# Optimization experiments

Measured on AMD Instinct MI355X. Metric: run time of the kernel, lower is better.

Reference implementation:

```python
import jax, jax.numpy as jnp
import numpy as np
import math

BN_EPS = 1e-5
LOG20 = math.log(20.0)

def conv1x1(w, x):
    # w: [O, C], x: [B, C, N] -> [B, O, N]
    return jnp.einsum('oc,bcn->bon', w, x)

def bn_silu(x, g, b, m, v):
    # inference-mode BatchNorm1d over channel dim, then SiLU
    y = (x - m[None, :, None]) * (g / jnp.sqrt(v + BN_EPS))[None, :, None] + b[None, :, None]
    return y * jax.nn.sigmoid(y)

def setup_inputs() -> dict:
    key = jax.random.key(0)
    ks = jax.random.split(key, 16)
    B, N, M = 8, 4096, 4096
    f32 = jnp.float32
    d = {
        'pcd_f': jax.random.normal(ks[0], (B, 1152, N), f32),
        'img_f': jax.random.normal(ks[1], (B, 1024, M), f32),
        'q_w': jax.random.normal(ks[2], (1024, 1152), f32) * 0.02,
        'k_w': jax.random.normal(ks[3], (1024, 1024), f32) * 0.02,
        'v_w': jax.random.normal(ks[4], (1024, 1024), f32) * 0.02,
        'skip_w': jax.random.normal(ks[5], (1024, 1152), f32) * 0.02,
        'c1_w': jax.random.normal(ks[6], (256, 1024), f32) * 0.03,
        'bn1_g': jnp.ones((256,), f32),
        'bn1_b': jnp.zeros((256,), f32),
        'bn1_m': jax.random.normal(ks[7], (256,), f32) * 0.1,
        'bn1_v': jnp.ones((256,), f32) + 0.1 * jax.random.uniform(ks[8], (256,)),
        'c2_w': jax.random.normal(ks[9], (64, 256), f32) * 0.06,
        'bn2_g': jnp.ones((64,), f32),
        'bn2_b': jnp.zeros((64,), f32),
        'bn2_m': jax.random.normal(ks[10], (64,), f32) * 0.1,
        'bn2_v': jnp.ones((64,), f32) + 0.1 * jax.random.uniform(ks[11], (64,)),
        'c3_w': jax.random.normal(ks[12], (1, 64), f32) * 0.1,
        'c3_b': jnp.zeros((1,), f32),
    }
    return d

def reference(pcd_f, img_f, q_w, k_w, v_w, skip_w, c1_w, bn1_g, bn1_b, bn1_m, bn1_v,
              c2_w, bn2_g, bn2_b, bn2_m, bn2_v, c3_w, c3_b):
    q = conv1x1(q_w, pcd_f)                       # [B, 1024, N]
    k = conv1x1(k_w, img_f)                       # [B, 1024, M]
    v = conv1x1(v_w, img_f)                       # [B, 1024, M]
    scale = math.sqrt(q.shape[1])                 # sqrt(C) = 32
    energy = jnp.einsum('bcn,bcm->bnm', q, k) / scale
    attn = jax.nn.softmax(energy, axis=-1)        # [B, N, M]
    x = jnp.einsum('bnm,bcm->bcn', attn, v)       # [B, 1024, N]
    x = conv1x1(skip_w, pcd_f) + x
    x = bn_silu(conv1x1(c1_w, x), bn1_g, bn1_b, bn1_m, bn1_v)   # [B, 256, N]
    x = bn_silu(conv1x1(c2_w, x), bn2_g, bn2_b, bn2_m, bn2_v)   # [B, 64, N]
    x = conv1x1(c3_w, x) + c3_b[None, :, None]    # [B, 1, N]
    x = x[:, 0, :]                                # squeeze channel -> [B, N]
    return jax.nn.sigmoid(x * LOG20)              # 1/(1+20^-x)
```

## Files before the change

### kernel.cpp

```cpp
#include <hip/hip_runtime.h>

#define LOG20F 2.9957322735539909f
#define AS1 __attribute__((address_space(1)))
#define AS3 __attribute__((address_space(3)))

typedef __attribute__((ext_vector_type(4))) short short4v;
typedef __attribute__((ext_vector_type(8))) short short8;
typedef __attribute__((ext_vector_type(8))) __bf16 bf16x8;
typedef __attribute__((ext_vector_type(4))) float f32x4;

__device__ __forceinline__ short f2bf(float f) {
  unsigned u = __float_as_uint(f);
  u = u + 0x7fffu + ((u >> 16) & 1u);
  return (short)(u >> 16);
}
__device__ __forceinline__ float bf2f(short s) {
  return __uint_as_float(((unsigned)(unsigned short)s) << 16);
}

__device__ __forceinline__ void xcd_map(int& bx, int& by, int& bz) {
  int gx = gridDim.x, gy = gridDim.y;
  int nwg = gx * gy * (int)gridDim.z;
  int lin = bx + gx * (by + gy * bz);
  int q = nwg >> 3, r = nwg & 7;
  int xcd = lin & 7, idx = lin >> 3;
  int wg = (xcd < r ? xcd * (q + 1) : r * (q + 1) + (xcd - r) * q) + idx;
  int per_z = gx * gy;
  bz = wg / per_z;
  int rz = wg - bz * per_z;
  if ((gx & 3) == 0 && (gy & 3) == 0) {
    int nstx = gx >> 2;
    int st = rz >> 4, w = rz & 15;
    bx = ((st % nstx) << 2) + (w & 3);
    by = ((st / nstx) << 2) + (w >> 2);
  } else {
    bx = rz % gx;
    by = rz / gx;
  }
}

template <int EPI>
__global__ __launch_bounds__(512, 2) void gemm8(
    const short* __restrict__ A, const short* __restrict__ B,
    short* __restrict__ C, const short* __restrict__ addp,
    int K, int lda, int ldb, int ldc, int ldadd,
    long abatch, long bbatch, long cbatch, long addbatch, float scale)
{
  __shared__ __align__(16) short lA[2][256 * 64];
  __shared__ __align__(16) short lB[2][256 * 64];

  int bx = blockIdx.x, by = blockIdx.y, bz = blockIdx.z;
  xcd_map(bx, by, bz);

  const int tid = threadIdx.x;
  const int lane = tid & 63, wid = tid >> 6;
  const int wr = wid >> 2, wc = wid & 3;

  const long bm = (long)bx * 256, bn = (long)by * 256;
  const short* Ab = A + (long)bz * abatch + bm * lda;
  const short* Bb = B + (long)bz * bbatch + bn * ldb;

  f32x4 acc[8][4] = {};

  const int NKT = K >> 6;

  auto stageA = [&](int buf, int kt) {
    int k0 = kt << 6;
#pragma unroll
    for (int i = 0; i < 4; ++i) {
      int idx = i * 512 + tid;
      int row = idx >> 3, ch = idx & 7;
      int chs = ch ^ (row & 7);
      __builtin_amdgcn_global_load_lds(
          (const AS1 void*)(Ab + (long)row * lda + k0 + chs * 8),
          (AS3 void*)(&lA[buf][row * 64 + ch * 8]), 16, 0, 0);
    }
  };
  auto stageB = [&](int buf, int kt) {
    int k0 = kt << 6;
#pragma unroll
    for (int i = 0; i < 4; ++i) {
      int idx = i * 512 + tid;
      int row = idx >> 3, ch = idx & 7;
      int chs = ch ^ (row & 7);
      __builtin_amdgcn_global_load_lds(
          (const AS1 void*)(Bb + (long)row * ldb + k0 + chs * 8),
          (AS3 void*)(&lB[buf][row * 64 + ch * 8]), 16, 0, 0);
    }
  };

  const int rr = lane & 15, cl = lane >> 4;
  bf16x8 bfr[4][2], af[4][2];

  auto loadA2 = [&](int buf, int h) {
#pragma unroll
    for (int f = 0; f < 4; ++f) {
      int row = wr * 128 + h * 64 + f * 16 + rr;
#pragma unroll
      for (int kk = 0; kk < 2; ++kk) {
        int pch = (kk * 4 + cl) ^ (row & 7);
        af[f][kk] = *(const bf16x8*)&lA[buf][row * 64 + pch * 8];
      }
    }
  };
  auto loadB2 = [&](int buf) {
#pragma unroll
    for (int ni = 0; ni < 4; ++ni) {
      int row = wc * 64 + ni * 16 + rr;
#pragma unroll
      for (int kk = 0; kk < 2; ++kk) {
        int pch = (kk * 4 + cl) ^ (row & 7);
        bfr[ni][kk] = *(const bf16x8*)&lB[buf][row * 64 + pch * 8];
      }
    }
  };

#define BAR() __builtin_amdgcn_s_barrier()
#define LGKM0() asm volatile("s_waitcnt lgkmcnt(0)" ::: "memory")
#define MFMA_H(h)                                                        \
  do {                                                                   \
    __builtin_amdgcn_s_setprio(1);                                       \
    _Pragma("unroll")                                                    \
    for (int f = 0; f < 4; ++f)                                          \
      _Pragma("unroll")                                                  \
      for (int ni = 0; ni < 4; ++ni)                                     \
        _Pragma("unroll")                                                \
        for (int kk = 0; kk < 2; ++kk)                                   \
          acc[(h) * 4 + f][ni] = __builtin_amdgcn_mfma_f32_16x16x32_bf16(\
              af[f][kk], bfr[ni][kk], acc[(h) * 4 + f][ni], 0, 0, 0);    \
    __builtin_amdgcn_s_setprio(0);                                       \
  } while (0)

  stageB(0, 0); stageA(0, 0); stageB(1, 1);
  asm volatile("s_waitcnt vmcnt(4)" ::: "memory");
  BAR();

  for (int t2 = 0; t2 < NKT; t2 += 2) {
    const bool more = (t2 + 2 < NKT);
    stageA(1, t2 + 1);
    loadB2(0); loadA2(0, 0);
    BAR(); LGKM0(); MFMA_H(0); BAR();
    if (more) stageB(0, t2 + 2);
    loadA2(0, 1);
    if (more) { asm volatile("s_waitcnt vmcnt(4)" ::: "memory"); }
    else      { asm volatile("s_waitcnt vmcnt(0)" ::: "memory"); }
    BAR(); LGKM0(); MFMA_H(1); BAR();
    if (more) stageA(0, t2 + 2);
    loadB2(1); loadA2(1, 0);
    BAR(); LGKM0(); MFMA_H(0); BAR();
    if (more) stageB(1, t2 + 3);
    loadA2(1, 1);
    if (more) { asm volatile("s_waitcnt vmcnt(4)" ::: "memory"); }
    else      { asm volatile("s_waitcnt vmcnt(0)" ::: "memory"); }
    BAR(); LGKM0(); MFMA_H(1); BAR();
  }
#undef BAR
#undef LGKM0
#undef MFMA_H

#pragma unroll
  for (int mi = 0; mi < 8; ++mi) {
    long row0 = bm + wr * 128 + (mi >> 2) * 64 + (mi & 3) * 16 + (cl << 2);
#pragma unroll
    for (int ni = 0; ni < 4; ++ni) {
      long col = bn + wc * 64 + ni * 16 + rr;
#pragma unroll
      for (int r = 0; r < 4; ++r) {
        long off = (long)bz * cbatch + (row0 + r) * ldc + col;
        float v = acc[mi][ni][r] * scale;
        if constexpr (EPI == 1)
          v += bf2f(addp[(long)bz * addbatch + (row0 + r) * ldadd + col]);
        C[off] = f2bf(v);
      }
    }
  }
}

__device__ __forceinline__ int swz32(int row, int ch) {
  return row * 32 + ((ch ^ ((row >> 1) & 3)) << 3);
}

template <int BM, int BN, int WR, int WC, int EPI>
__global__ __launch_bounds__(WR * WC * 64, 4) void gemm_bt(
    const short* __restrict__ A, const short* __restrict__ B,
    short* __restrict__ C, const short* __restrict__ addp,
    const float* __restrict__ sc, const float* __restrict__ sh,
    int K, int lda, int ldb, int ldc,
    long abatch, long bbatch, long cbatch, float scale)
{
  constexpr int NTH = WR * WC * 64;
  constexpr int WM = BM / WR, WN = BN / WC;
  constexpr int MR = WM / 16, NR = WN / 16;
  constexpr int CA = (BM * 4) / NTH, CB = (BN * 4) / NTH;

  __shared__ __align__(16) short lA[2][BM * 32];
  __shared__ __align__(16) short lB[2][BN * 32];

  int bx = blockIdx.x, by = blockIdx.y, bz = blockIdx.z;
  xcd_map(bx, by, bz);

  const int tid = threadIdx.x;
  const int lane = tid & 63, wid = tid >> 6;
  const int wr = wid / WC, wc = wid % WC;

  const long bm = (long)bx * BM, bn = (long)by * BN;
  const short* Ab = A + (long)bz * abatch + bm * lda;
  const short* Bb = B + (long)bz * bbatch + bn * ldb;

  f32x4 acc[MR][NR] = {};

  auto stage = [&](int buf, int k0) {
#pragma unroll
    for (int i = 0; i < CA; ++i) {
      int idx = i * NTH + tid, row = idx >> 2, ch = idx & 3;
      int chs = ch ^ ((row >> 1) & 3);
      __builtin_amdgcn_global_load_lds(
          (const AS1 void*)(Ab + (long)row * lda + k0 + chs * 8),
          (AS3 void*)(&lA[buf][idx * 8]), 16, 0, 0);
    }
#pragma unroll
    for (int i = 0; i < CB; ++i) {
      int idx = i * NTH + tid, row = idx >> 2, ch = idx & 3;
      int chs = ch ^ ((row >> 1) & 3);
      __builtin_amdgcn_global_load_lds(
          (const AS1 void*)(Bb + (long)row * ldb + k0 + chs * 8),
          (AS3 void*)(&lB[buf][idx * 8]), 16, 0, 0);
    }
  };

  const int NT = K >> 5;
  stage(0, 0);
  __syncthreads();
  int cur = 0;
  for (int t = 0; t < NT; ++t) {
    if (t + 1 < NT) stage(cur ^ 1, (t + 1) << 5);
    const int ch = lane >> 4, rrow = lane & 15;
    bf16x8 af[MR], bfr[NR];
#pragma unroll
    for (int mi = 0; mi < MR; ++mi) {
      int row = wr * WM + mi * 16 + rrow;
      af[mi] = *(const bf16x8*)&lA[cur][swz32(row, ch)];
    }
#pragma unroll
    for (int ni = 0; ni < NR; ++ni) {
      int row = wc * WN + ni * 16 + rrow;
      bfr[ni] = *(const bf16x8*)&lB[cur][swz32(row, ch)];
    }
    __builtin_amdgcn_s_setprio(1);
#pragma unroll
    for (int mi = 0; mi < MR; ++mi)
#pragma unroll
      for (int ni = 0; ni < NR; ++ni)
        acc[mi][ni] = __builtin_amdgcn_mfma_f32_16x16x32_bf16(
            af[mi], bfr[ni], acc[mi][ni], 0, 0, 0);
    __builtin_amdgcn_s_setprio(0);
    __syncthreads();
    cur ^= 1;
  }

#pragma unroll
  for (int mi = 0; mi < MR; ++mi) {
    long row0 = bm + wr * WM + mi * 16 + ((lane >> 4) << 2);
#pragma unroll
    for (int ni = 0; ni < NR; ++ni) {
      long col = bn + wc * WN + ni * 16 + (lane & 15);
#pragma unroll
      for (int r = 0; r < 4; ++r) {
        long off = (long)bz * cbatch + (row0 + r) * ldc + col;
        float v = acc[mi][ni][r] * scale;
        if constexpr (EPI == 1) v += bf2f(addp[off]);
        if constexpr (EPI == 2) {
          float y = v * sc[col] + sh[col];
          v = y / (1.f + __expf(-y));
        }
        C[off] = f2bf(v);
      }
    }
  }
}

__global__ __launch_bounds__(256) void transpose_cvt(
    const float* __restrict__ in, short* __restrict__ out, int C, int N)
{
  __shared__ float tile[32][33];
  int n0 = blockIdx.x * 32, c0 = blockIdx.y * 32;
  long z = (long)blockIdx.z * C * N;
  int tx = threadIdx.x & 31, ty = threadIdx.x >> 5;
#pragma unroll
  for (int r = 0; r < 4; ++r) {
    int cc = ty + r * 8;
    tile[cc][tx] = in[z + (long)(c0 + cc) * N + n0 + tx];
  }
  __syncthreads();
#pragma unroll
  for (int r = 0; r < 4; ++r) {
    int nn = ty + r * 8;
    out[z + (long)(n0 + nn) * C + c0 + tx] = f2bf(tile[tx][nn]);
  }
}

__global__ __launch_bounds__(256) void cvt_bf16(
    const float* __restrict__ in, short* __restrict__ out, long n)
{
  long i = ((long)blockIdx.x * 256 + threadIdx.x) * 4;
  if (i >= n) return;
  const float* p = in + i;
  short4v s;
  s[0] = f2bf(p[0]); s[1] = f2bf(p[1]); s[2] = f2bf(p[2]); s[3] = f2bf(p[3]);
  *(short4v*)(out + i) = s;
}

__global__ void bn_prep(const float* g1, const float* b1, const float* m1, const float* v1,
                        const float* g2, const float* b2, const float* m2, const float* v2,
                        float* s1, float* t1, float* s2, float* t2)
{
  int i = threadIdx.x;
  if (i < 256) { float s = g1[i] * rsqrtf(v1[i] + 1e-5f); s1[i] = s; t1[i] = b1[i] - m1[i] * s; }
  if (i < 64)  { float s = g2[i] * rsqrtf(v2[i] + 1e-5f); s2[i] = s; t2[i] = b2[i] - m2[i] * s; }
}

__global__ __launch_bounds__(256) void softmax_row(short* __restrict__ a)
{
  __shared__ float rm[4], rs[4];
  long row = blockIdx.x;
  short* p = a + row * 4096;
  int tid = threadIdx.x;
  short8 v0 = *(short8*)(p + tid * 16);
  short8 v1 = *(short8*)(p + tid * 16 + 8);
  float f[16];
#pragma unroll
  for (int j = 0; j < 8; ++j) { f[j] = bf2f(v0[j]); f[8 + j] = bf2f(v1[j]); }
  float m = f[0];
#pragma unroll
  for (int j = 1; j < 16; ++j) m = fmaxf(m, f[j]);
  for (int o = 32; o > 0; o >>= 1) m = fmaxf(m, __shfl_xor(m, o));
  if ((tid & 63) == 0) rm[tid >> 6] = m;
  __syncthreads();
  m = fmaxf(fmaxf(rm[0], rm[1]), fmaxf(rm[2], rm[3]));
  float s = 0.f;
#pragma unroll
  for (int j = 0; j < 16; ++j) { f[j] = __expf(f[j] - m); s += f[j]; }
  for (int o = 32; o > 0; o >>= 1) s += __shfl_xor(s, o);
  if ((tid & 63) == 0) rs[tid >> 6] = s;
  __syncthreads();
  s = rs[0] + rs[1] + rs[2] + rs[3];
  float inv = 1.f / s;
#pragma unroll
  for (int j = 0; j < 8; ++j) { v0[j] = f2bf(f[j] * inv); v1[j] = f2bf(f[8 + j] * inv); }
  *(short8*)(p + tid * 16) = v0;
  *(short8*)(p + tid * 16 + 8) = v1;
}

__global__ __launch_bounds__(256) void c3_out(
    const short* __restrict__ y2, const float* __restrict__ w,
    const float* __restrict__ bias, float* __restrict__ o, int total)
{
  int i = blockIdx.x * 256 + threadIdx.x;
  if (i >= total) return;
  const short8* r = (const short8*)(y2 + (long)i * 64);
  float acc = 0.f;
#pragma unroll
  for (int j0 = 0; j0 < 8; ++j0) {
    short8 v = r[j0];
#pragma unroll
    for (int j = 0; j < 8; ++j) acc += bf2f(v[j]) * w[j0 * 8 + j];
  }
  acc += bias[0];
  float x = acc * LOG20F;
  o[i] = 1.f / (1.f + __expf(-x));
}

extern "C" void kernel_launch(void* const* d_in, const int* in_sizes, int n_in,
                              void* d_out, int out_size, void* d_ws, size_t ws_size,
                              hipStream_t stream) {
  const float* pcd  = (const float*)d_in[0];
  const float* img  = (const float*)d_in[1];
  const float* qw   = (const float*)d_in[2];
  const float* kw   = (const float*)d_in[3];
  const float* vw   = (const float*)d_in[4];
  const float* skw  = (const float*)d_in[5];
  const float* c1w  = (const float*)d_in[6];
  const float* bn1g = (const float*)d_in[7];
  const float* bn1b = (const float*)d_in[8];
  const float* bn1m = (const float*)d_in[9];
  const float* bn1v = (const float*)d_in[10];
  const float* c2w  = (const float*)d_in[11];
  const float* bn2g = (const float*)d_in[12];
  const float* bn2b = (const float*)d_in[13];
  const float* bn2m = (const float*)d_in[14];
  const float* bn2v = (const float*)d_in[15];
  const float* c3w  = (const float*)d_in[16];
  const float* c3b  = (const float*)d_in[17];
  float* out = (float*)d_out;

  char* ws = (char*)d_ws;
  const long QS  = 4096L * 1024;
  const long QS2 = 4096L * 2048;
  const long ES  = 4096L * 4096;
  const size_t ALGN = 256;
  auto align_up = [&](size_t x) { return (x + ALGN - 1) & ~(ALGN - 1); };

  size_t oPcd  = 0;
  size_t oImg  = align_up(oPcd + 8L * 4096 * 1152 * 2);
  size_t oQsk  = align_up(oImg + 8L * 4096 * 1024 * 2);
  size_t oKt   = align_up(oQsk + 8L * QS2 * 2);
  size_t oV    = align_up(oKt  + 8L * QS * 2);
  size_t oWqs  = align_up(oV   + 8L * QS * 2);
  size_t oWk   = align_up(oWqs + 2048L * 1152 * 2);
  size_t oWv   = align_up(oWk + 1024L * 1024 * 2);
  size_t oC1   = align_up(oWv + 1024L * 1024 * 2);
  size_t oC2   = align_up(oC1 + 256L * 1024 * 2);
  size_t oS1   = align_up(oC2 + 64L * 256 * 2);
  size_t oT1   = align_up(oS1 + 256 * 4);
  size_t oS2   = align_up(oT1 + 256 * 4);
  size_t oT2   = align_up(oS2 + 64 * 4);
  size_t oEnd  = align_up(oT2 + 64 * 4);

  short* pcdT  = (short*)(ws + oPcd);
  short* imgT  = (short*)(ws + oImg);
  short* qsk   = (short*)(ws + oQsk);
  short* kt    = (short*)(ws + oKt);
  short* vbuf  = (short*)(ws + oV);
  short* wqsk  = (short*)(ws + oWqs);
  short* wkb   = (short*)(ws + oWk);
  short* wvb   = (short*)(ws + oWv);
  short* c1b   = (short*)(ws + oC1);
  short* c2b   = (short*)(ws + oC2);
  float* s1 = (float*)(ws + oS1); float* t1 = (float*)(ws + oT1);
  float* s2 = (float*)(ws + oS2); float* t2 = (float*)(ws + oT2);

  int NB; short *attn, *xt;
  if (ws_size >= oEnd + (size_t)(8L * ES * 2) + (size_t)(8L * QS * 2)) {
    NB = 8; attn = (short*)(ws + oEnd); xt = (short*)(ws + align_up(oEnd + 8L * ES * 2));
  } else if (ws_size >= oEnd + (size_t)(8L * QS * 2)) {
    NB = 4; attn = (short*)(ws + 0); xt = (short*)(ws + oEnd);
  } else {
    NB = 2; attn = imgT; xt = pcdT;
  }
  short* y1t = qsk;
  short* y2t = kt;

  cvt_bf16<<<dim3(1152), 256, 0, stream>>>(qw,  wqsk,                 1024L * 1152);
  cvt_bf16<<<dim3(1152), 256, 0, stream>>>(skw, wqsk + 1024L * 1152,  1024L * 1152);
  cvt_bf16<<<dim3(1024), 256, 0, stream>>>(kw,  wkb,  1024L * 1024);
  cvt_bf16<<<dim3(1024), 256, 0, stream>>>(vw,  wvb,  1024L * 1024);
  cvt_bf16<<<dim3(256),  256, 0, stream>>>(c1w, c1b,  256L * 1024);
  cvt_bf16<<<dim3(16),   256, 0, stream>>>(c2w, c2b,  64L * 256);
  bn_prep<<<1, 256, 0, stream>>>(bn1g, bn1b, bn1m, bn1v, bn2g, bn2b, bn2m, bn2v,
                                 s1, t1, s2, t2);
  transpose_cvt<<<dim3(128, 36, 8), 256, 0, stream>>>(pcd, pcdT, 1152, 4096);
  transpose_cvt<<<dim3(128, 32, 8), 256, 0, stream>>>(img, imgT, 1024, 4096);

  gemm8<0><<<dim3(16, 8, 8), 512, 0, stream>>>(
      pcdT, wqsk, qsk, nullptr,
      1152, 1152, 1152, 2048, 0, 4096L * 1152, 0, QS2, 0, 1.f);
  gemm8<0><<<dim3(16, 4, 8), 512, 0, stream>>>(
      imgT, wkb, kt, nullptr,
      1024, 1024, 1024, 1024, 0, QS, 0, QS, 0, 1.f);
  gemm8<0><<<dim3(4, 16, 8), 512, 0, stream>>>(
      wvb, imgT, vbuf, nullptr,
      1024, 1024, 1024, 4096, 0, 0, QS, QS, 0, 1.f);

  for (int b0 = 0; b0 < 8; b0 += NB) {
    gemm8<0><<<dim3(16, 16, NB), 512, 0, stream>>>(
        qsk + (long)b0 * QS2, kt + (long)b0 * QS, attn, nullptr,
        1024, 2048, 1024, 4096, 0, QS2, QS, ES, 0, 0.03125f);
    softmax_row<<<dim3(4096 * NB), 256, 0, stream>>>(attn);
    gemm8<1><<<dim3(16, 4, NB), 512, 0, stream>>>(
        attn, vbuf + (long)b0 * QS, xt + (long)b0 * QS,
        qsk + (long)b0 * QS2 + 1024,
        4096, 4096, 4096, 1024, 2048, ES, QS, QS, QS2, 1.f);
  }

  gemm_bt<128, 128, 2, 2, 2><<<dim3(32, 2, 8), 256, 0, stream>>>(
      xt, c1b, y1t, nullptr, s1, t1,
      1024, 1024, 1024, 256, QS, 0, 4096L * 256, 1.f);
  gemm_bt<128, 64, 4, 1, 2><<<dim3(32, 1, 8), 256, 0, stream>>>(
      y1t, c2b, y2t, nullptr, s2, t2,
      256, 256, 256, 64, 4096L * 256, 0, 4096L * 64, 1.f);
  c3_out<<<dim3(128), 256, 0, stream>>>(y2t, c3w, c3b, out, 32768);

  (void)in_sizes; (void)n_in; (void)out_size; (void)ws_size;
}
```

Measured before the change: 1.111 ms.

## Fuse softmax into QK and PV GEMM epilogues and pad leading dimensions

Drops the separate softmax kernel. The QK^T GEMM epilogue now writes exp(scaled energy) and adds row sums into a global buffer through shared and global atomics, and the PV GEMM divides by the row sum in its epilogue. This saves a full read and write pass over the attention matrix. The max subtraction is skipped, which relies on the logits staying small enough not to overflow. Leading dimensions are also padded (e.g. 4128, 1056, 2080) to avoid LDS and channel conflicts, and the NB=8 path is removed so batches are always processed in chunks.

```diff
diff --git a/kernel.cpp b/kernel.cpp
--- a/kernel.cpp
+++ b/kernel.cpp
@@ -43,11 +43,13 @@
 __global__ __launch_bounds__(512, 2) void gemm8(
     const short* __restrict__ A, const short* __restrict__ B,
     short* __restrict__ C, const short* __restrict__ addp,
+    float* __restrict__ rs,
     int K, int lda, int ldb, int ldc, int ldadd,
     long abatch, long bbatch, long cbatch, long addbatch, float scale)
 {
   __shared__ __align__(16) short lA[2][256 * 64];
   __shared__ __align__(16) short lB[2][256 * 64];
+  __shared__ float rsum_l[256];
 
   int bx = blockIdx.x, by = blockIdx.y, bz = blockIdx.z;
   xcd_map(bx, by, bz);
@@ -158,19 +160,49 @@
 #undef LGKM0
 #undef MFMA_H
 
-#pragma unroll
-  for (int mi = 0; mi < 8; ++mi) {
-    long row0 = bm + wr * 128 + (mi >> 2) * 64 + (mi & 3) * 16 + (cl << 2);
-#pragma unroll
-    for (int ni = 0; ni < 4; ++ni) {
-      long col = bn + wc * 64 + ni * 16 + rr;
+  if constexpr (EPI == 2) {
+    if (tid < 256) rsum_l[tid] = 0.f;
+    __syncthreads();
+#pragma unroll
+    for (int mi = 0; mi < 8; ++mi) {
+      int lrow0 = wr * 128 + (mi >> 2) * 64 + (mi & 3) * 16 + (cl << 2);
 #pragma unroll
       for (int r = 0; r < 4; ++r) {
-        long off = (long)bz * cbatch + (row0 + r) * ldc + col;
-        float v = acc[mi][ni][r] * scale;
-        if constexpr (EPI == 1)
-          v += bf2f(addp[(long)bz * addbatch + (row0 + r) * ldadd + col]);
-        C[off] = f2bf(v);
+        float part = 0.f;
+#pragma unroll
+        for (int ni = 0; ni < 4; ++ni) {
+          long col = bn + wc * 64 + ni * 16 + rr;
+          float e = __expf(acc[mi][ni][r] * scale);
+          C[(long)bz * cbatch + (bm + lrow0 + r) * ldc + col] = f2bf(e);
+          part += e;
+        }
+        atomicAdd(&rsum_l[lrow0 + r], part);
+      }
+    }
+    __syncthreads();
+    if (tid < 256) atomicAdd(&rs[(long)bz * 4096 + bm + tid], rsum_l[tid]);
+  } else {
+#pragma unroll
+    for (int mi = 0; mi < 8; ++mi) {
+      long row0 = bm + wr * 128 + (mi >> 2) * 64 + (mi & 3) * 16 + (cl << 2);
+      float inv[4];
+      if constexpr (EPI == 1) {
+#pragma unroll
+        for (int r = 0; r < 4; ++r)
+          inv[r] = 1.f / rs[(long)bz * 4096 + row0 + r];
+      }
+#pragma unroll
+      for (int ni = 0; ni < 4; ++ni) {
+        long col = bn + wc * 64 + ni * 16 + rr;
+#pragma unroll
+        for (int r = 0; r < 4; ++r) {
+          long off = (long)bz * cbatch + (row0 + r) * ldc + col;
+          float v = acc[mi][ni][r] * scale;
+          if constexpr (EPI == 1)
+            v = v * inv[r] +
+                bf2f(addp[(long)bz * addbatch + (row0 + r) * ldadd + col]);
+          C[off] = f2bf(v);
+        }
       }
     }
   }
@@ -280,22 +312,23 @@
 }
 
 __global__ __launch_bounds__(256) void transpose_cvt(
-    const float* __restrict__ in, short* __restrict__ out, int C, int N)
+    const float* __restrict__ in, short* __restrict__ out, int C, int N, int ldo)
 {
   __shared__ float tile[32][33];
   int n0 = blockIdx.x * 32, c0 = blockIdx.y * 32;
-  long z = (long)blockIdx.z * C * N;
+  long zi = (long)blockIdx.z * C * N;
+  long zo = (long)blockIdx.z * (long)N * ldo;
   int tx = threadIdx.x & 31, ty = threadIdx.x >> 5;
 #pragma unroll
   for (int r = 0; r < 4; ++r) {
     int cc = ty + r * 8;
-    tile[cc][tx] = in[z + (long)(c0 + cc) * N + n0 + tx];
+    tile[cc][tx] = in[zi + (long)(c0 + cc) * N + n0 + tx];
   }
   __syncthreads();
 #pragma unroll
   for (int r = 0; r < 4; ++r) {
     int nn = ty + r * 8;
-    out[z + (long)(n0 + nn) * C + c0 + tx] = f2bf(tile[tx][nn]);
+    out[zo + (long)(n0 + nn) * ldo + c0 + tx] = f2bf(tile[tx][nn]);
   }
 }
 
@@ -319,36 +352,10 @@
   if (i < 64)  { float s = g2[i] * rsqrtf(v2[i] + 1e-5f); s2[i] = s; t2[i] = b2[i] - m2[i] * s; }
 }
 
-__global__ __launch_bounds__(256) void softmax_row(short* __restrict__ a)
-{
-  __shared__ float rm[4], rs[4];
-  long row = blockIdx.x;
-  short* p = a + row * 4096;
-  int tid = threadIdx.x;
-  short8 v0 = *(short8*)(p + tid * 16);
-  short8 v1 = *(short8*)(p + tid * 16 + 8);
-  float f[16];
-#pragma unroll
-  for (int j = 0; j < 8; ++j) { f[j] = bf2f(v0[j]); f[8 + j] = bf2f(v1[j]); }
-  float m = f[0];
-#pragma unroll
-  for (int j = 1; j < 16; ++j) m = fmaxf(m, f[j]);
-  for (int o = 32; o > 0; o >>= 1) m = fmaxf(m, __shfl_xor(m, o));
-  if ((tid & 63) == 0) rm[tid >> 6] = m;
-  __syncthreads();
-  m = fmaxf(fmaxf(rm[0], rm[1]), fmaxf(rm[2], rm[3]));
-  float s = 0.f;
-#pragma unroll
-  for (int j = 0; j < 16; ++j) { f[j] = __expf(f[j] - m); s += f[j]; }
-  for (int o = 32; o > 0; o >>= 1) s += __shfl_xor(s, o);
-  if ((tid & 63) == 0) rs[tid >> 6] = s;
-  __syncthreads();
-  s = rs[0] + rs[1] + rs[2] + rs[3];
-  float inv = 1.f / s;
-#pragma unroll
-  for (int j = 0; j < 8; ++j) { v0[j] = f2bf(f[j] * inv); v1[j] = f2bf(f[8 + j] * inv); }
-  *(short8*)(p + tid * 16) = v0;
-  *(short8*)(p + tid * 16 + 8) = v1;
+__global__ __launch_bounds__(256) void zerof(float* __restrict__ p, int n)
+{
+  int i = blockIdx.x * 256 + threadIdx.x;
+  if (i < n) p[i] = 0.f;
 }
 
 __global__ __launch_bounds__(256) void c3_out(
@@ -393,19 +400,22 @@
   const float* c3b  = (const float*)d_in[17];
   float* out = (float*)d_out;
 
+  const int QLD = 2080, KLD = 1056, ALD = 4128, VLD = 4128, Y1LD = 288;
+  const long QS2 = 4096L * QLD;
+  const long QS  = 4096L * KLD;
+  const long VBS = 1024L * VLD;
+  const long ES  = 4096L * ALD;
+
   char* ws = (char*)d_ws;
-  const long QS  = 4096L * 1024;
-  const long QS2 = 4096L * 2048;
-  const long ES  = 4096L * 4096;
   const size_t ALGN = 256;
   auto align_up = [&](size_t x) { return (x + ALGN - 1) & ~(ALGN - 1); };
 
   size_t oPcd  = 0;
   size_t oImg  = align_up(oPcd + 8L * 4096 * 1152 * 2);
-  size_t oQsk  = align_up(oImg + 8L * 4096 * 1024 * 2);
+  size_t oQsk  = align_up(oImg + 8L * 4096 * KLD * 2);
   size_t oKt   = align_up(oQsk + 8L * QS2 * 2);
   size_t oV    = align_up(oKt  + 8L * QS * 2);
-  size_t oWqs  = align_up(oV   + 8L * QS * 2);
+  size_t oWqs  = align_up(oV   + 8L * VBS * 2);
   size_t oWk   = align_up(oWqs + 2048L * 1152 * 2);
   size_t oWv   = align_up(oWk + 1024L * 1024 * 2);
   size_t oC1   = align_up(oWv + 1024L * 1024 * 2);
@@ -414,7 +424,8 @@
   size_t oT1   = align_up(oS1 + 256 * 4);
   size_t oS2   = align_up(oT1 + 256 * 4);
   size_t oT2   = align_up(oS2 + 64 * 4);
-  size_t oEnd  = align_up(oT2 + 64 * 4);
+  size_t oRs   = align_up(oT2 + 64 * 4);
+  size_t oEnd  = align_up(oRs + 8L * 4096 * 4);
 
   short* pcdT  = (short*)(ws + oPcd);
   short* imgT  = (short*)(ws + oImg);
@@ -428,56 +439,57 @@
   short* c2b   = (short*)(ws + oC2);
   float* s1 = (float*)(ws + oS1); float* t1 = (float*)(ws + oT1);
   float* s2 = (float*)(ws + oS2); float* t2 = (float*)(ws + oT2);
+  float* rsum = (float*)(ws + oRs);
 
   int NB; short *attn, *xt;
-  if (ws_size >= oEnd + (size_t)(8L * ES * 2) + (size_t)(8L * QS * 2)) {
-    NB = 8; attn = (short*)(ws + oEnd); xt = (short*)(ws + align_up(oEnd + 8L * ES * 2));
-  } else if (ws_size >= oEnd + (size_t)(8L * QS * 2)) {
+  if (ws_size >= oEnd + (size_t)(8L * QS * 2)) {
     NB = 4; attn = (short*)(ws + 0); xt = (short*)(ws + oEnd);
   } else {
-    NB = 2; attn = imgT; xt = pcdT;
+    NB = 2; attn = (short*)(ws + 0);
+    xt = (short*)(ws + align_up((size_t)(2L * ES * 2)));
   }
   short* y1t = qsk;
   short* y2t = kt;
 
-  cvt_bf16<<<dim3(1152), 256, 0, stream>>>(qw,  wqsk,                 1024L * 1152);
-  cvt_bf16<<<dim3(1152), 256, 0, stream>>>(skw, wqsk + 1024L * 1152,  1024L * 1152);
+  cvt_bf16<<<dim3(1152), 256, 0, stream>>>(qw,  wqsk,                1024L * 1152);
+  cvt_bf16<<<dim3(1152), 256, 0, stream>>>(skw, wqsk + 1024L * 1152, 1024L * 1152);
   cvt_bf16<<<dim3(1024), 256, 0, stream>>>(kw,  wkb,  1024L * 1024);
   cvt_bf16<<<dim3(1024), 256, 0, stream>>>(vw,  wvb,  1024L * 1024);
   cvt_bf16<<<dim3(256),  256, 0, stream>>>(c1w, c1b,  256L * 1024);
   cvt_bf16<<<dim3(16),   256, 0, stream>>>(c2w, c2b,  64L * 256);
   bn_prep<<<1, 256, 0, stream>>>(bn1g, bn1b, bn1m, bn1v, bn2g, bn2b, bn2m, bn2v,
                                  s1, t1, s2, t2);
-  transpose_cvt<<<dim3(128, 36, 8), 256, 0, stream>>>(pcd, pcdT, 1152, 4096);
-  transpose_cvt<<<dim3(128, 32, 8), 256, 0, stream>>>(img, imgT, 1024, 4096);
+  zerof<<<dim3(128), 256, 0, stream>>>(rsum, 8 * 4096);
+  transpose_cvt<<<dim3(128, 36, 8), 256, 0, stream>>>(pcd, pcdT, 1152, 4096, 1152);
+  transpose_cvt<<<dim3(128, 32, 8), 256, 0, stream>>>(img, imgT, 1024, 4096, KLD);
 
   gemm8<0><<<dim3(16, 8, 8), 512, 0, stream>>>(
-      pcdT, wqsk, qsk, nullptr,
-      1152, 1152, 1152, 2048, 0, 4096L * 1152, 0, QS2, 0, 1.f);
+      pcdT, wqsk, qsk, nullptr, nullptr,
+      1152, 1152, 1152, QLD, 0, 4096L * 1152, 0, QS2, 0, 1.f);
   gemm8<0><<<dim3(16, 4, 8), 512, 0, stream>>>(
-      imgT, wkb, kt, nullptr,
-      1024, 1024, 1024, 1024, 0, QS, 0, QS, 0, 1.f);
+      imgT, wkb, kt, nullptr, nullptr,
+      1024, KLD, 1024, KLD, 0, QS, 0, QS, 0, 1.f);
   gemm8<0><<<dim3(4, 16, 8), 512, 0, stream>>>(
-      wvb, imgT, vbuf, nullptr,
-      1024, 1024, 1024, 4096, 0, 0, QS, QS, 0, 1.f);
+      wvb, imgT, vbuf, nullptr, nullptr,
+      1024, 1024, KLD, VLD, 0, 0, QS, VBS, 0, 1.f);
 
   for (int b0 = 0; b0 < 8; b0 += NB) {
-    gemm8<0><<<dim3(16, 16, NB), 512, 0, stream>>>(
+    gemm8<2><<<dim3(16, 16, NB), 512, 0, stream>>>(
         qsk + (long)b0 * QS2, kt + (long)b0 * QS, attn, nullptr,
-        1024, 2048, 1024, 4096, 0, QS2, QS, ES, 0, 0.03125f);
-    softmax_row<<<dim3(4096 * NB), 256, 0, stream>>>(attn);
+        rsum + (long)b0 * 4096,
+        1024, QLD, KLD, ALD, 0, QS2, QS, ES, 0, 0.03125f);
     gemm8<1><<<dim3(16, 4, NB), 512, 0, stream>>>(
-        attn, vbuf + (long)b0 * QS, xt + (long)b0 * QS,
-        qsk + (long)b0 * QS2 + 1024,
-        4096, 4096, 4096, 1024, 2048, ES, QS, QS, QS2, 1.f);
+        attn, vbuf + (long)b0 * VBS, xt + (long)b0 * QS,
+        qsk + (long)b0 * QS2 + 1024, rsum + (long)b0 * 4096,
+        4096, ALD, VLD, KLD, QLD, ES, VBS, QS, QS2, 1.f);
   }
 
   gemm_bt<128, 128, 2, 2, 2><<<dim3(32, 2, 8), 256, 0, stream>>>(
       xt, c1b, y1t, nullptr, s1, t1,
-      1024, 1024, 1024, 256, QS, 0, 4096L * 256, 1.f);
+      1024, KLD, 1024, Y1LD, QS, 0, 4096L * Y1LD, 1.f);
   gemm_bt<128, 64, 4, 1, 2><<<dim3(32, 1, 8), 256, 0, stream>>>(
       y1t, c2b, y2t, nullptr, s2, t2,
-      256, 256, 256, 64, 4096L * 256, 0, 4096L * 64, 1.f);
+      256, Y1LD, 256, 64, 4096L * Y1LD, 0, 4096L * 64, 1.f);
   c3_out<<<dim3(128), 256, 0, stream>>>(y2t, c3w, c3b, out, 32768);
 
   (void)in_sizes; (void)n_in; (void)out_size; (void)ws_size;
```

Result: slower. 1.255 ms (+13.0%).
